# Kernel tuning notes

Measured on AMD Instinct MI355X. Metric: run time of the kernel, lower is better.

## Reference

```python
import jax, jax.numpy as jnp
import numpy as np

NUM_GROUPS = 4194304  # 2^22 groups
GROUP_SIZE = 32
PACKED_GROUP_SIZE = GROUP_SIZE // 2 + 1  # 16 data bytes + 1 scale byte


def setup_inputs() -> dict:
    key = jax.random.key(0)
    packed = jax.random.randint(key, (NUM_GROUPS * PACKED_GROUP_SIZE,), 0, 256, dtype=jnp.int32)
    return {"packed": packed, "group_size": GROUP_SIZE, "ebits": 2, "mbits": 1}


def reference(packed, group_size, ebits, mbits):
    # MX4 -> fp32 dequantization: unpack 4-bit nibbles + per-group exp2 scale.
    packed_group_size = group_size // 2 + 1
    num_groups = packed.shape[0] // packed_group_size
    clamp_max = 2 ** (2 ** ebits - 1)                      # 8 for ebits=2
    max_val = clamp_max * (2.0 - 2.0 ** (-mbits))          # 12.0 for mbits=1

    pg = packed.reshape(num_groups, packed_group_size)
    # last byte of each group is the shared scale exponent (biased by 127)
    log_scale = jnp.clip(pg[:, -1].astype(jnp.float32) - 127.0, -126.0, 127.0)
    group_scale = jnp.exp2(log_scale)                      # (num_groups,)

    data = pg[:, : group_size // 2]                        # (num_groups, group_size//2)
    low = (data & 15).astype(jnp.float32)
    high = ((data >> 4) & 15).astype(jnp.float32)
    # interleave low/high nibbles: element order [low0, high0, low1, high1, ...]
    unpacked = jnp.stack([low, high], axis=-1).reshape(num_groups, group_size)
    unpacked = unpacked - jnp.float32(clamp_max)

    out = unpacked / jnp.float32(max_val) * group_scale[:, None]
    return out.reshape(-1).astype(jnp.float32)
```

## Files before the change

### kernel.cpp

```cpp
#include <hip/hip_runtime.h>


constexpr int kGroupSize = 32;
constexpr int kPGS = kGroupSize / 2 + 1;

constexpr int kBlock = 256;
constexpr int kGroupsPerBlock = 256;
constexpr int kTileWords = kGroupsPerBlock * kPGS;
constexpr int kVec4PerBlock = kGroupsPerBlock * kGroupSize / 4;
constexpr int kChunkWords = 256;
constexpr int kChunks = kTileWords / kChunkWords;

__global__ __launch_bounds__(kBlock) void dequant_mxfp4_lds_kernel(
    const int* __restrict__ packed,
    const int* __restrict__ ebits_p,
    const int* __restrict__ mbits_p,
    float* __restrict__ out)
{
    __shared__ int tile[kTileWords];

    const int t    = threadIdx.x;
    const int wave = t >> 6;
    const int lane = t & 63;

    const int* gsrc = packed + (size_t)blockIdx.x * kTileWords;

#pragma unroll
    for (int k = 0; k < 5; ++k) {
        const int c = k * 4 + wave;
        if (c < kChunks) {
            const int* g = gsrc + c * kChunkWords + lane * 4;
            __builtin_amdgcn_global_load_lds(
                (const __attribute__((address_space(1))) int*)g,
                (__attribute__((address_space(3))) int*)&tile[c * kChunkWords],
                16 , 0, 0);
        }
    }

    const int ebits = ebits_p[0];
    const int mbits = mbits_p[0];
    const float clamp_max = (float)(1 << ((1 << ebits) - 1));
    const float inv_max   = 1.0f / (clamp_max * (2.0f - exp2f((float)(-mbits))));

    __syncthreads();

    float4* outv = reinterpret_cast<float4*>(out) + (size_t)blockIdx.x * kVec4PerBlock;

#pragma unroll
    for (int k = 0; k < kVec4PerBlock / kBlock; ++k) {
        const int v    = t + kBlock * k;
        const int g    = v >> 3;
        const int b0   = (v & 7) * 2;
        const int base = g * kPGS;

        const int w0 = tile[base + b0];
        const int w1 = tile[base + b0 + 1];
        const int s  = tile[base + kGroupSize / 2];

        int e = s - 127;
        e = min(max(e, -126), 127);
        const float coef = ldexpf(1.0f, e) * inv_max;

        float4 r;
        r.x = ((float)(w0 & 15)        - clamp_max) * coef;
        r.y = ((float)((w0 >> 4) & 15) - clamp_max) * coef;
        r.z = ((float)(w1 & 15)        - clamp_max) * coef;
        r.w = ((float)((w1 >> 4) & 15) - clamp_max) * coef;

        outv[v] = r;
    }
}

__global__ __launch_bounds__(256) void dequant_mxfp4_tail_kernel(
    const int* __restrict__ packed,
    const int* __restrict__ ebits_p,
    const int* __restrict__ mbits_p,
    float* __restrict__ out,
    int v_begin, int n_vec4)
{
    int v = v_begin + blockIdx.x * 256 + threadIdx.x;
    if (v >= n_vec4) return;

    const int ebits = ebits_p[0];
    const int mbits = mbits_p[0];
    const float clamp_max = (float)(1 << ((1 << ebits) - 1));
    const float inv_max   = 1.0f / (clamp_max * (2.0f - exp2f((float)(-mbits))));

    int g  = v >> 3;
    int b0 = (v & 7) * 2;
    int base = g * kPGS;

    int w0 = packed[base + b0];
    int w1 = packed[base + b0 + 1];
    int s  = packed[base + kGroupSize / 2];

    int e = s - 127;
    e = min(max(e, -126), 127);
    float coef = ldexpf(1.0f, e) * inv_max;

    float4 r;
    r.x = ((float)(w0 & 15)        - clamp_max) * coef;
    r.y = ((float)((w0 >> 4) & 15) - clamp_max) * coef;
    r.z = ((float)(w1 & 15)        - clamp_max) * coef;
    r.w = ((float)((w1 >> 4) & 15) - clamp_max) * coef;

    reinterpret_cast<float4*>(out)[v] = r;
}

extern "C" void kernel_launch(void* const* d_in, const int* in_sizes, int n_in,
                              void* d_out, int out_size, void* d_ws, size_t ws_size,
                              hipStream_t stream) {
    const int* packed  = (const int*)d_in[0];
    const int* ebits_p = (const int*)d_in[2];
    const int* mbits_p = (const int*)d_in[3];
    float* out = (float*)d_out;

    const int n_vec4 = out_size / 4;
    const int n_full = n_vec4 / kVec4PerBlock;
    const int tail   = n_vec4 - n_full * kVec4PerBlock;

    if (n_full > 0) {
        dequant_mxfp4_lds_kernel<<<n_full, kBlock, 0, stream>>>(
            packed, ebits_p, mbits_p, out);
    }
    if (tail > 0) {
        const int tgrid = (tail + 255) / 256;
        dequant_mxfp4_tail_kernel<<<tgrid, 256, 0, stream>>>(
            packed, ebits_p, mbits_p, out, n_full * kVec4PerBlock, n_vec4);
    }
}
```

Measured before the change: 699.3 us.

## Make dequant kernel persistent with double-buffered LDS staging and nontemporal stores

Replaces the one-tile-per-block launch with a fixed grid of 1024 persistent blocks that loop over tiles. Each block prefetches the next tile into a second LDS buffer with global_load_lds while it dequantizes the current one, so input loads overlap compute. Output writes become nontemporal vector stores to reduce cache pollution. The trade-offs are doubled LDS per block, fewer resident blocks, and dependence on the compiler waiting for the async LDS loads before the barrier.

```diff
diff --git a/kernel.cpp b/kernel.cpp
--- a/kernel.cpp
+++ b/kernel.cpp
@@ -5,26 +5,18 @@
 constexpr int kPGS = kGroupSize / 2 + 1;
 
 constexpr int kBlock = 256;
-constexpr int kGroupsPerBlock = 256;
-constexpr int kTileWords = kGroupsPerBlock * kPGS;
-constexpr int kVec4PerBlock = kGroupsPerBlock * kGroupSize / 4;
+constexpr int kGroupsPerTile = 256;
+constexpr int kTileWords = kGroupsPerTile * kPGS;
+constexpr int kVec4PerTile = kGroupsPerTile * kGroupSize / 4;
 constexpr int kChunkWords = 256;
 constexpr int kChunks = kTileWords / kChunkWords;
+constexpr int kGrid = 1024;
 
-__global__ __launch_bounds__(kBlock) void dequant_mxfp4_lds_kernel(
-    const int* __restrict__ packed,
-    const int* __restrict__ ebits_p,
-    const int* __restrict__ mbits_p,
-    float* __restrict__ out)
+typedef float vfloat4 __attribute__((ext_vector_type(4)));
+
+__device__ __forceinline__ void stage_tile(const int* __restrict__ gsrc,
+                                           int* ldst, int wave, int lane)
 {
-    __shared__ int tile[kTileWords];
-
-    const int t    = threadIdx.x;
-    const int wave = t >> 6;
-    const int lane = t & 63;
-
-    const int* gsrc = packed + (size_t)blockIdx.x * kTileWords;
-
 #pragma unroll
     for (int k = 0; k < 5; ++k) {
         const int c = k * 4 + wave;
@@ -32,27 +24,21 @@
             const int* g = gsrc + c * kChunkWords + lane * 4;
             __builtin_amdgcn_global_load_lds(
                 (const __attribute__((address_space(1))) int*)g,
-                (__attribute__((address_space(3))) int*)&tile[c * kChunkWords],
+                (__attribute__((address_space(3))) int*)(ldst + c * kChunkWords),
                 16 , 0, 0);
         }
     }
+}
 
-    const int ebits = ebits_p[0];
-    const int mbits = mbits_p[0];
-    const float clamp_max = (float)(1 << ((1 << ebits) - 1));
-    const float inv_max   = 1.0f / (clamp_max * (2.0f - exp2f((float)(-mbits))));
-
-    __syncthreads();
-
-    float4* outv = reinterpret_cast<float4*>(out) + (size_t)blockIdx.x * kVec4PerBlock;
-
+__device__ __forceinline__ void compute_tile(const int* __restrict__ tile,
+                                             vfloat4* __restrict__ outv,
+                                             int t, float clamp_max, float inv_max)
+{
+    const int gb = (t >> 3) * kPGS;
+    const int b0 = (t & 7) * 2;
 #pragma unroll
-    for (int k = 0; k < kVec4PerBlock / kBlock; ++k) {
-        const int v    = t + kBlock * k;
-        const int g    = v >> 3;
-        const int b0   = (v & 7) * 2;
-        const int base = g * kPGS;
-
+    for (int k = 0; k < kVec4PerTile / kBlock; ++k) {
+        const int base = gb + k * 32 * kPGS;
         const int w0 = tile[base + b0];
         const int w1 = tile[base + b0 + 1];
         const int s  = tile[base + kGroupSize / 2];
@@ -61,13 +47,51 @@
         e = min(max(e, -126), 127);
         const float coef = ldexpf(1.0f, e) * inv_max;
 
-        float4 r;
+        vfloat4 r;
         r.x = ((float)(w0 & 15)        - clamp_max) * coef;
         r.y = ((float)((w0 >> 4) & 15) - clamp_max) * coef;
         r.z = ((float)(w1 & 15)        - clamp_max) * coef;
         r.w = ((float)((w1 >> 4) & 15) - clamp_max) * coef;
 
-        outv[v] = r;
+        __builtin_nontemporal_store(r, &outv[t + kBlock * k]);
+    }
+}
+
+__global__ __launch_bounds__(kBlock) void dequant_mxfp4_v3_kernel(
+    const int* __restrict__ packed,
+    const int* __restrict__ ebits_p,
+    const int* __restrict__ mbits_p,
+    float* __restrict__ out,
+    int n_tiles)
+{
+    __shared__ int tile[2][kTileWords];
+
+    const int t    = threadIdx.x;
+    const int wave = t >> 6;
+    const int lane = t & 63;
+
+    int ti = blockIdx.x;
+    if (ti >= n_tiles) return;
+
+    const int ebits = ebits_p[0];
+    const int mbits = mbits_p[0];
+    const float clamp_max = (float)(1 << ((1 << ebits) - 1));
+    const float inv_max   = 1.0f / (clamp_max * (2.0f - exp2f((float)(-mbits))));
+
+    stage_tile(packed + (size_t)ti * kTileWords, tile[0], wave, lane);
+
+    int buf = 0;
+    for (; ti < n_tiles; ti += kGrid) {
+        __syncthreads();
+
+        const int tn = ti + kGrid;
+        if (tn < n_tiles)
+            stage_tile(packed + (size_t)tn * kTileWords, tile[buf ^ 1], wave, lane);
+
+        compute_tile(tile[buf],
+                     reinterpret_cast<vfloat4*>(out) + (size_t)ti * kVec4PerTile,
+                     t, clamp_max, inv_max);
+        buf ^= 1;
     }
 }
 
@@ -115,17 +139,18 @@
     const int* mbits_p = (const int*)d_in[3];
     float* out = (float*)d_out;
 
-    const int n_vec4 = out_size / 4;
-    const int n_full = n_vec4 / kVec4PerBlock;
-    const int tail   = n_vec4 - n_full * kVec4PerBlock;
+    const int n_vec4  = out_size / 4;
+    const int n_tiles = n_vec4 / kVec4PerTile;
+    const int tail    = n_vec4 - n_tiles * kVec4PerTile;
 
-    if (n_full > 0) {
-        dequant_mxfp4_lds_kernel<<<n_full, kBlock, 0, stream>>>(
-            packed, ebits_p, mbits_p, out);
+    if (n_tiles > 0) {
+        const int grid = n_tiles < kGrid ? n_tiles : kGrid;
+        dequant_mxfp4_v3_kernel<<<grid, kBlock, 0, stream>>>(
+            packed, ebits_p, mbits_p, out, n_tiles);
     }
     if (tail > 0) {
         const int tgrid = (tail + 255) / 256;
         dequant_mxfp4_tail_kernel<<<tgrid, 256, 0, stream>>>(
-            packed, ebits_p, mbits_p, out, n_full * kVec4PerBlock, n_vec4);
+            packed, ebits_p, mbits_p, out, n_tiles * kVec4PerTile, n_vec4);
     }
 }
```

New measurement: 719.0 us. 1.03x slower.
